# Optimization experiments

Hardware: AMD Instinct MI355X
Metric: run time of the kernel (lower is better)

Reference implementation:

```python
import jax, jax.numpy as jnp
import numpy as np

N = 50000      # number of nodes (rows of edge_embeddings)
E = 800000     # number of edges
D = 256        # edge_dim
TOPK = 50


def setup_inputs() -> dict:
    key = jax.random.key(0)
    k1, k2, k3, k4, k5, k6 = jax.random.split(key, 6)
    edge_embeddings = jax.random.normal(k1, (N, D), dtype=jnp.float32)
    edge_index = jax.random.randint(k2, (2, E), 0, N, dtype=jnp.int64)
    # PyTorch nn.Linear default init: U(-1/sqrt(fan_in), 1/sqrt(fan_in))
    s1 = 1.0 / np.sqrt(2 * D)
    s2 = 1.0 / np.sqrt(D)
    W1 = jax.random.uniform(k3, (2 * D, D), jnp.float32, -s1, s1)
    b1 = jax.random.uniform(k4, (D,), jnp.float32, -s1, s1)
    W2 = jax.random.uniform(k5, (D, 1), jnp.float32, -s2, s2)
    b2 = jax.random.uniform(k6, (1,), jnp.float32, -s2, s2)
    return {"edge_embeddings": edge_embeddings, "W1": W1, "b1": b1,
            "W2": W2, "b2": b2, "edge_index": edge_index, "top_k": TOPK}


def reference(edge_embeddings, W1, b1, W2, b2, edge_index, top_k):
    src, dst = edge_index[0], edge_index[1]           # [E]
    valid = src < dst                                  # original keeps only i<j pairs
    # gather + concat: [E, 2D]
    pair_emb = jnp.concatenate([edge_embeddings[src], edge_embeddings[dst]], axis=-1)
    h = jax.nn.relu(pair_emb @ W1 + b1)                # [E, D]
    score = jax.nn.sigmoid(h @ W2 + b2)[:, 0]          # [E], in (0,1)
    # invalid edges get score -1 (< any sigmoid output) so topk picks only valid ones
    masked = jnp.where(valid, score, jnp.float32(-1.0))
    top_scores, top_idx = jax.lax.top_k(masked, top_k)
    top_pairs = edge_index[:, top_idx]                 # [2, k] (src,dst) of top edges
    return top_pairs, top_scores
```

## Files before the change

### kernel.cpp

```cpp
#include <hip/hip_runtime.h>
#include <hip/hip_bf16.h>
#include <cstdint>

#define TOPK 50
#define CANDS 400
#define HIST_BINS 16384
#define CAND_CAP 16384
#define NFBLK 512
#define SORT_CAP 8192

typedef __attribute__((ext_vector_type(8))) short bf16x8;
typedef __attribute__((ext_vector_type(4))) float f32x4;

__device__ __forceinline__ unsigned short f2bf(float f) {
    unsigned u = __float_as_uint(f);
    u += 0x7FFFu + ((u >> 16) & 1u);
    return (unsigned short)(u >> 16);
}

__global__ __launch_bounds__(256) void prep_count(const float* __restrict__ W1,
                                                  unsigned* __restrict__ Wcf4,
                                                  unsigned* __restrict__ hist,
                                                  unsigned* __restrict__ misc,
                                                  const int* __restrict__ eidx,
                                                  unsigned* __restrict__ bcount, int E) {
    __shared__ int s_is64;
    if (threadIdx.x == 0) {
        int allz = 1;
        for (int q = 0; q < 64; ++q)
            if (eidx[2 * q + 1] != 0) { allz = 0; break; }
        s_is64 = allz;
    }
    __syncthreads();
    const int is64 = s_is64;

    int g = blockIdx.x * blockDim.x + threadIdx.x;
    if (g < 256 * 64) {
        int l = g & 63;
        int kt = (g >> 6) & 7;
        int nt = g >> 9;
        int col = nt * 16 + (l & 15);
        int kb = kt * 32 + (l >> 4) * 8;
        unsigned short h[8];
#pragma unroll
        for (int j = 0; j < 8; ++j) {
            int k = kb + j;
            float f = (col < 256) ? W1[k * 256 + col] : W1[(256 + k) * 256 + (col - 256)];
            h[j] = f2bf(f);
        }
        unsigned* dst = Wcf4 + (size_t)g * 4;
        dst[0] = (unsigned)h[0] | ((unsigned)h[1] << 16);
        dst[1] = (unsigned)h[2] | ((unsigned)h[3] << 16);
        dst[2] = (unsigned)h[4] | ((unsigned)h[5] << 16);
        dst[3] = (unsigned)h[6] | ((unsigned)h[7] << 16);
    }
    if (g < HIST_BINS) hist[g] = 0;
    if (g == 0) {
        misc[0] = (unsigned)is64;
        misc[2] = 0;
        misc[3] = 0;
        misc[4] = 0;
    }

    const int chunk = (E + gridDim.x - 1) / gridDim.x;
    const int lo = blockIdx.x * chunk;
    const int hi = min(E, lo + chunk);
    unsigned cnt = 0;
    for (int e = lo + threadIdx.x; e < hi; e += blockDim.x) {
        int s, d;
        if (is64) {
            s = ((const int2*)eidx)[e].x;
            d = ((const int2*)eidx)[(size_t)e + E].x;
        } else {
            s = eidx[e];
            d = eidx[e + E];
        }
        cnt += (s < d);
    }
#pragma unroll
    for (int off = 32; off; off >>= 1) cnt += __shfl_xor(cnt, off, 64);
    __shared__ unsigned wsum[4];
    if ((threadIdx.x & 63) == 0) wsum[threadIdx.x >> 6] = cnt;
    __syncthreads();
    if (threadIdx.x == 0)
        bcount[blockIdx.x] = wsum[0] + wsum[1] + wsum[2] + wsum[3];
}

__global__ __launch_bounds__(256) void gemm_fused(const float* __restrict__ emb,
                                                  const bf16x8* __restrict__ Bv,
                                                  const float* __restrict__ b1,
                                                  unsigned char* __restrict__ C8, int M) {
    __shared__ uint4 afrag[2048];
    const int t = threadIdx.x;
    const int w = t >> 6;
    const int l = t & 63;

    uint2* w2 = (uint2*)afrag;
#pragma unroll
    for (int iter = 0; iter < 16; ++iter) {
        int r = iter * 4 + w;
        int c0 = l * 4;
        int gr = blockIdx.x * 64 + r;
        float4 v = make_float4(0.f, 0.f, 0.f, 0.f);
        if (gr < M) v = *(const float4*)&emb[(size_t)gr * 256 + c0];
        unsigned u0 = (unsigned)f2bf(v.x) | ((unsigned)f2bf(v.y) << 16);
        unsigned u1 = (unsigned)f2bf(v.z) | ((unsigned)f2bf(v.w) << 16);
        int mt = r >> 4;
        int kt = c0 >> 5;
        int lane = (r & 15) + ((c0 & 31) >> 3) * 16;
        int f = mt * 8 + kt;
        int slot = f * 64 + (lane ^ (f & 7));
        w2[slot * 2 + ((c0 & 7) >> 2)] = make_uint2(u0, u1);
    }
    __syncthreads();

    const int wn = w;
#pragma unroll
    for (int nh = 0; nh < 2; ++nh) {
        f32x4 acc[4][4];
#pragma unroll
        for (int i = 0; i < 4; ++i)
#pragma unroll
            for (int j = 0; j < 4; ++j) acc[i][j] = (f32x4){0.f, 0.f, 0.f, 0.f};

        const int nt0 = wn * 8 + nh * 4;
        bf16x8 bcur[4];
#pragma unroll
        for (int j = 0; j < 4; ++j)
            bcur[j] = Bv[(size_t)((nt0 + j) * 8 + 0) * 64 + l];

#pragma unroll
        for (int kt = 0; kt < 8; ++kt) {
            bf16x8 af[4];
#pragma unroll
            for (int i = 0; i < 4; ++i)
                af[i] = *(const bf16x8*)&afrag[(i * 8 + kt) * 64 + (l ^ kt)];
            bf16x8 bnxt[4];
            if (kt < 7) {
#pragma unroll
                for (int j = 0; j < 4; ++j)
                    bnxt[j] = Bv[(size_t)((nt0 + j) * 8 + kt + 1) * 64 + l];
            }
#pragma unroll
            for (int i = 0; i < 4; ++i)
#pragma unroll
                for (int j = 0; j < 4; ++j)
                    acc[i][j] = __builtin_amdgcn_mfma_f32_16x16x32_bf16(af[i], bcur[j], acc[i][j], 0, 0, 0);
            if (kt < 7) {
#pragma unroll
                for (int j = 0; j < 4; ++j) bcur[j] = bnxt[j];
            }
        }

#pragma unroll
        for (int i = 0; i < 4; ++i) {
            int row0 = blockIdx.x * 64 + i * 16 + (l >> 4) * 4;
#pragma unroll
            for (int j = 0; j < 4; ++j) {
                int col = (nt0 + j) * 16 + (l & 15);
                float bias = (col < 256) ? b1[col] : 0.f;
#pragma unroll
                for (int r = 0; r < 4; ++r) {
                    float v = acc[i][j][r] + bias;
                    int pk = __builtin_amdgcn_cvt_pk_fp8_f32(v, v, 0, false);
                    C8[(size_t)(row0 + r) * 512 + col] = (unsigned char)(pk & 0xFF);
                }
            }
        }
    }
}

__global__ __launch_bounds__(256) void write_valid_scan(const int* __restrict__ eidx,
                                                        unsigned* __restrict__ misc,
                                                        const unsigned* __restrict__ bcount,
                                                        int* __restrict__ vsrc,
                                                        int* __restrict__ vdst,
                                                        int* __restrict__ vid, int E) {
    const int is64 = (int)misc[0];
    const int bid = blockIdx.x;
    const int t = threadIdx.x;
    __shared__ unsigned red[256];

    unsigned c0 = bcount[t], c1 = bcount[t + 256];
    unsigned pa = ((t < bid) ? c0 : 0u) + ((t + 256 < bid) ? c1 : 0u);
    red[t] = pa;
    __syncthreads();
    for (int s = 128; s; s >>= 1) {
        if (t < s) red[t] += red[t + s];
        __syncthreads();
    }
    const unsigned myoff = red[0];
    __syncthreads();
    red[t] = c0 + c1;
    __syncthreads();
    for (int s = 128; s; s >>= 1) {
        if (t < s) red[t] += red[t + s];
        __syncthreads();
    }
    if (bid == 0 && t == 0) misc[4] = red[0];

    const int chunk = (E + gridDim.x - 1) / gridDim.x;
    const int lo = bid * chunk;
    const int hi = min(E, lo + chunk);
    const int lane = t & 63;
    const int w = t >> 6;
    __shared__ unsigned wcnt[4];
    unsigned running = myoff;
    for (int base = lo; base < hi; base += blockDim.x) {
        int e = base + t;
        bool valid = false;
        int s = 0, d = 0;
        if (e < hi) {
            if (is64) {
                s = ((const int2*)eidx)[e].x;
                d = ((const int2*)eidx)[(size_t)e + E].x;
            } else {
                s = eidx[e];
                d = eidx[e + E];
            }
            valid = s < d;
        }
        unsigned long long m = __ballot(valid);
        unsigned pfx = __popcll(m & ((1ull << lane) - 1ull));
        if (lane == 0) wcnt[w] = __popcll(m);
        __syncthreads();
        unsigned wbase = running;
        for (int i = 0; i < w; ++i) wbase += wcnt[i];
        if (valid) {
            unsigned p = wbase + pfx;
            vsrc[p] = s;
            vdst[p] = d;
            vid[p] = e;
        }
        unsigned tot = wcnt[0] + wcnt[1] + wcnt[2] + wcnt[3];
        __syncthreads();
        running += tot;
    }
}

__device__ __forceinline__ float dotq(unsigned a, unsigned b, float4 w) {
    float s;
    s  = fmaxf(__builtin_amdgcn_cvt_f32_fp8(a, 0) + __builtin_amdgcn_cvt_f32_fp8(b, 0), 0.f) * w.x;
    s += fmaxf(__builtin_amdgcn_cvt_f32_fp8(a, 1) + __builtin_amdgcn_cvt_f32_fp8(b, 1), 0.f) * w.y;
    s += fmaxf(__builtin_amdgcn_cvt_f32_fp8(a, 2) + __builtin_amdgcn_cvt_f32_fp8(b, 2), 0.f) * w.z;
    s += fmaxf(__builtin_amdgcn_cvt_f32_fp8(a, 3) + __builtin_amdgcn_cvt_f32_fp8(b, 3), 0.f) * w.w;
    return s;
}

__global__ __launch_bounds__(256) void edge_score_fp8(const unsigned char* __restrict__ C8,
                                                      const int* __restrict__ vsrc,
                                                      const int* __restrict__ vdst,
                                                      const float* __restrict__ W2,
                                                      const float* __restrict__ b2,
                                                      float* __restrict__ svals,
                                                      const unsigned* __restrict__ misc) {
    const int V = (int)misc[4];
    const int lane = threadIdx.x & 63;
    const int q = lane & 15;
    const int g = lane >> 4;
    const int wid = blockIdx.x * (blockDim.x >> 6) + (threadIdx.x >> 6);
    const int nw = gridDim.x * (blockDim.x >> 6);

    const float4 w0 = *(const float4*)&W2[q * 16 + 0];
    const float4 w1 = *(const float4*)&W2[q * 16 + 4];
    const float4 w2 = *(const float4*)&W2[q * 16 + 8];
    const float4 w3 = *(const float4*)&W2[q * 16 + 12];
    const float bb2 = b2[0];

    for (int base = wid * 4; base < V; base += nw * 4) {
        const int slot = base + g;
        const bool ok = slot < V;
        const int src = ok ? vsrc[slot] : 0;
        const int dst = ok ? vdst[slot] : 0;
        const uint4 ua = *(const uint4*)(C8 + (size_t)src * 512 + q * 16);
        const uint4 ub = *(const uint4*)(C8 + (size_t)dst * 512 + 256 + q * 16);
        float p = dotq(ua.x, ub.x, w0);
        p += dotq(ua.y, ub.y, w1);
        p += dotq(ua.z, ub.z, w2);
        p += dotq(ua.w, ub.w, w3);
        p += __shfl_xor(p, 1, 64);
        p += __shfl_xor(p, 2, 64);
        p += __shfl_xor(p, 4, 64);
        p += __shfl_xor(p, 8, 64);
        if (q == 0 && ok) {
            float z = p + bb2;
            float sc = 1.0f / (1.0f + expf(-z));
            svals[slot] = sc;
        }
    }
}

__global__ __launch_bounds__(256) void hist_kernel(const float* __restrict__ svals,
                                                   const unsigned* __restrict__ misc,
                                                   unsigned* __restrict__ hist) {
    __shared__ unsigned lh[HIST_BINS];
    const int V = (int)misc[4];
    const int t = threadIdx.x;
    for (int i = t; i < HIST_BINS; i += 256) lh[i] = 0;
    __syncthreads();
    int i = blockIdx.x * blockDim.x + t;
    int stride = gridDim.x * blockDim.x;
    for (int v = i; v < V; v += stride)
        atomicAdd(&lh[__float_as_uint(svals[v]) >> 16], 1u);
    __syncthreads();
    for (int b = t; b < HIST_BINS; b += 256) {
        unsigned c = lh[b];
        if (c) atomicAdd(&hist[b], c);
    }
}

__global__ __launch_bounds__(256) void compact(const float* __restrict__ svals,
                                               const int* __restrict__ vid,
                                               const unsigned* __restrict__ hist,
                                               unsigned* __restrict__ misc,
                                               unsigned long long* __restrict__ cand) {
    __shared__ unsigned chunk[256];
    __shared__ unsigned s_thr;
    const int t = threadIdx.x;
    {
        unsigned s = 0;
        for (int i = 0; i < 64; ++i) s += hist[t * 64 + i];
        chunk[t] = s;
    }
    __syncthreads();
    if (t == 0) {
        unsigned cum = 0;
        int c;
        unsigned thr = 0;
        for (c = 255; c >= 0; --c) {
            if (cum + chunk[c] >= CANDS) break;
            cum += chunk[c];
        }
        if (c >= 0) {
            for (int b = c * 64 + 63; b >= c * 64; --b) {
                cum += hist[b];
                if (cum >= CANDS) { thr = ((unsigned)b) << 16; break; }
            }
        }
        s_thr = thr;
    }
    __syncthreads();
    const unsigned thr = s_thr;

    const int V = (int)misc[4];
    int i = blockIdx.x * blockDim.x + t;
    int stride = gridDim.x * blockDim.x;
    for (int v = i; v < V; v += stride) {
        unsigned bits = __float_as_uint(svals[v]);
        if (bits >= thr) {
            unsigned pos = atomicAdd(&misc[3], 1u);
            if (pos < CAND_CAP)
                cand[pos] = ((unsigned long long)bits << 32) |
                            (unsigned)(0xFFFFFFFFu - (unsigned)vid[v]);
        }
    }
}

__global__ __launch_bounds__(256) void rescore(const float* __restrict__ emb,
                                               const float* __restrict__ W1,
                                               const float* __restrict__ b1,
                                               const float* __restrict__ W2,
                                               const float* __restrict__ b2,
                                               const int* __restrict__ eidx,
                                               const unsigned long long* __restrict__ cand,
                                               const unsigned* __restrict__ misc,
                                               unsigned long long* __restrict__ rescored,
                                               int E) {
    __shared__ float es[256], ed[256];
    __shared__ float red[256];
    const int C = (int)min(misc[3], (unsigned)CAND_CAP);
    const int is64 = (int)misc[0];
    const int t = threadIdx.x;
    for (int c = blockIdx.x; c < C; c += gridDim.x) {
        unsigned long long entry = cand[c];
        unsigned e = 0xFFFFFFFFu - (unsigned)(entry & 0xFFFFFFFFu);
        int src, dst;
        if (is64) {
            src = eidx[2 * (size_t)e];
            dst = eidx[2 * ((size_t)e + E)];
        } else {
            src = eidx[e];
            dst = eidx[e + E];
        }
        es[t] = emb[(size_t)src * 256 + t];
        ed[t] = emb[(size_t)dst * 256 + t];
        __syncthreads();
        float h = b1[t];
#pragma unroll 8
        for (int k = 0; k < 256; ++k) h += es[k] * W1[k * 256 + t];
#pragma unroll 8
        for (int k = 0; k < 256; ++k) h += ed[k] * W1[(256 + k) * 256 + t];
        red[t] = fmaxf(h, 0.f) * W2[t];
        __syncthreads();
        for (int s = 128; s; s >>= 1) {
            if (t < s) red[t] += red[t + s];
            __syncthreads();
        }
        if (t == 0) {
            float z = red[0] + b2[0];
            float sc = 1.0f / (1.0f + expf(-z));
            rescored[c] = ((unsigned long long)__float_as_uint(sc) << 32) |
                          (unsigned)(0xFFFFFFFFu - e);
        }
        __syncthreads();
    }
}

__global__ __launch_bounds__(256) void final_topk(unsigned long long* __restrict__ rescored,
                                                  const unsigned* __restrict__ misc,
                                                  const int* __restrict__ eidx,
                                                  float* __restrict__ out, int E) {
    __shared__ unsigned long long a[SORT_CAP];
    const int t = threadIdx.x;
    const int C = (int)min(misc[3], (unsigned)CAND_CAP);
    const int is64 = (int)misc[0];

    if (C <= SORT_CAP) {
        int n = 256;
        while (n < C) n <<= 1;
        for (int i = t; i < n; i += 256) a[i] = (i < C) ? rescored[i] : 0ull;
        __syncthreads();
        for (int k = 2; k <= n; k <<= 1) {
            for (int j = k >> 1; j > 0; j >>= 1) {
                for (int i = t; i < n; i += 256) {
                    int ixj = i ^ j;
                    if (ixj > i) {
                        unsigned long long x = a[i], y = a[ixj];
                        bool sw = ((i & k) == 0) ? (x < y) : (x > y);
                        if (sw) { a[i] = y; a[ixj] = x; }
                    }
                }
                __syncthreads();
            }
        }
        if (t < TOPK) {
            unsigned long long m = a[t];
            if (m != 0ull) {
                unsigned bits = (unsigned)(m >> 32);
                unsigned e = 0xFFFFFFFFu - (unsigned)(m & 0xFFFFFFFFu);
                int src, dst;
                if (is64) {
                    src = eidx[2 * (size_t)e];
                    dst = eidx[2 * ((size_t)e + E)];
                } else {
                    src = eidx[e];
                    dst = eidx[e + E];
                }
                out[t] = (float)src;
                out[TOPK + t] = (float)dst;
                out[2 * TOPK + t] = __uint_as_float(bits);
            } else {
                out[t] = -1.f;
                out[TOPK + t] = -1.f;
                out[2 * TOPK + t] = -1.f;
            }
        }
        return;
    }

    __shared__ unsigned long long red[256];
    for (int r = 0; r < TOPK; ++r) {
        unsigned long long best = 0ull;
        for (int i = t; i < C; i += 256) {
            unsigned long long v = rescored[i];
            if (v > best) best = v;
        }
        red[t] = best;
        __syncthreads();
        for (int s = 128; s; s >>= 1) {
            if (t < s) {
                if (red[t + s] > red[t]) red[t] = red[t + s];
            }
            __syncthreads();
        }
        unsigned long long m = red[0];
        __syncthreads();
        for (int i = t; i < C; i += 256)
            if (rescored[i] == m) rescored[i] = 0ull;
        if (t == 0) {
            if (m != 0ull) {
                unsigned bits = (unsigned)(m >> 32);
                unsigned e = 0xFFFFFFFFu - (unsigned)(m & 0xFFFFFFFFu);
                int src, dst;
                if (is64) {
                    src = eidx[2 * (size_t)e];
                    dst = eidx[2 * ((size_t)e + E)];
                } else {
                    src = eidx[e];
                    dst = eidx[e + E];
                }
                out[r] = (float)src;
                out[TOPK + r] = (float)dst;
                out[2 * TOPK + r] = __uint_as_float(bits);
            } else {
                out[r] = -1.f;
                out[TOPK + r] = -1.f;
                out[2 * TOPK + r] = -1.f;
            }
        }
        __syncthreads();
    }
}

extern "C" void kernel_launch(void* const* d_in, const int* in_sizes, int n_in,
                              void* d_out, int out_size, void* d_ws, size_t ws_size,
                              hipStream_t stream) {
    const float* emb = (const float*)d_in[0];
    const float* W1  = (const float*)d_in[1];
    const float* b1  = (const float*)d_in[2];
    const float* W2  = (const float*)d_in[3];
    const float* b2  = (const float*)d_in[4];
    const int*   eidx = (const int*)d_in[5];

    const int M = in_sizes[0] / 256;
    const int E = in_sizes[5] / 2;
    const int Mpad = ((M + 63) / 64) * 64;

    char* p = (char*)d_ws;
    auto alloc = [&](size_t bytes) {
        char* r = p;
        p += (bytes + 255) & ~(size_t)255;
        return r;
    };
    unsigned* Wcf4 = (unsigned*)alloc(256 * 512 * 2);
    unsigned char* C8 = (unsigned char*)alloc((size_t)Mpad * 512);
    float* svals = (float*)alloc((size_t)E * 4);
    int* vsrc = (int*)alloc((size_t)E * 4);
    int* vdst = (int*)alloc((size_t)E * 4);
    int* vid  = (int*)alloc((size_t)E * 4);
    unsigned* hist = (unsigned*)alloc(HIST_BINS * 4);
    unsigned long long* cand = (unsigned long long*)alloc(CAND_CAP * 8);
    unsigned long long* resc = (unsigned long long*)alloc(CAND_CAP * 8);
    unsigned* bcount = (unsigned*)alloc(NFBLK * 4);
    unsigned* misc = (unsigned*)alloc(256);

    float* out = (float*)d_out;

    prep_count<<<NFBLK, 256, 0, stream>>>(W1, Wcf4, hist, misc, eidx, bcount, E);

    gemm_fused<<<Mpad / 64, 256, 0, stream>>>(emb, (const bf16x8*)Wcf4, b1, C8, M);

    write_valid_scan<<<NFBLK, 256, 0, stream>>>(eidx, misc, bcount, vsrc, vdst, vid, E);

    edge_score_fp8<<<2048, 256, 0, stream>>>(C8, vsrc, vdst, W2, b2, svals, misc);

    hist_kernel<<<128, 256, 0, stream>>>(svals, misc, hist);

    compact<<<512, 256, 0, stream>>>(svals, vid, hist, misc, cand);

    rescore<<<1024, 256, 0, stream>>>(emb, W1, b1, W2, b2, eidx, cand, misc, resc, E);

    final_topk<<<1, 256, 0, stream>>>(resc, misc, eidx, out, E);
}
```

Before: 150.8 us.

## Merge GEMM and valid-edge scan into one launch; subsample score histogram

Combines the bf16 MFMA GEMM and the valid-edge compaction scan into a single launch, with the first blocks doing the GEMM and the rest doing the scan. This removes one kernel launch and lets the two independent stages overlap. The histogram now samples every 8th score and uses a threshold rank of 64 among the samples instead of 400 among all scores, which cuts histogram atomic work. The cost is that the candidate threshold becomes statistical, so the candidate count varies and could overflow the cap or miss true top-k entries if the sampling is unrepresentative.

```diff
diff --git a/kernel.cpp b/kernel.cpp
--- a/kernel.cpp
+++ b/kernel.cpp
@@ -3,7 +3,8 @@
 #include <cstdint>
 
 #define TOPK 50
-#define CANDS 400
+#define SUB_RANK 64
+#define HIST_STRIDE 8
 #define HIST_BINS 16384
 #define CAND_CAP 16384
 #define NFBLK 512
@@ -86,155 +87,157 @@
         bcount[blockIdx.x] = wsum[0] + wsum[1] + wsum[2] + wsum[3];
 }
 
-__global__ __launch_bounds__(256) void gemm_fused(const float* __restrict__ emb,
-                                                  const bf16x8* __restrict__ Bv,
-                                                  const float* __restrict__ b1,
-                                                  unsigned char* __restrict__ C8, int M) {
+__global__ __launch_bounds__(256) void gemm_plus_write(const float* __restrict__ emb,
+                                                       const bf16x8* __restrict__ Bv,
+                                                       const float* __restrict__ b1,
+                                                       unsigned char* __restrict__ C8,
+                                                       int M, int NG,
+                                                       const int* __restrict__ eidx,
+                                                       unsigned* __restrict__ misc,
+                                                       const unsigned* __restrict__ bcount,
+                                                       int* __restrict__ vsrc,
+                                                       int* __restrict__ vdst,
+                                                       int* __restrict__ vid, int E) {
     __shared__ uint4 afrag[2048];
     const int t = threadIdx.x;
-    const int w = t >> 6;
-    const int l = t & 63;
-
-    uint2* w2 = (uint2*)afrag;
-#pragma unroll
-    for (int iter = 0; iter < 16; ++iter) {
-        int r = iter * 4 + w;
-        int c0 = l * 4;
-        int gr = blockIdx.x * 64 + r;
-        float4 v = make_float4(0.f, 0.f, 0.f, 0.f);
-        if (gr < M) v = *(const float4*)&emb[(size_t)gr * 256 + c0];
-        unsigned u0 = (unsigned)f2bf(v.x) | ((unsigned)f2bf(v.y) << 16);
-        unsigned u1 = (unsigned)f2bf(v.z) | ((unsigned)f2bf(v.w) << 16);
-        int mt = r >> 4;
-        int kt = c0 >> 5;
-        int lane = (r & 15) + ((c0 & 31) >> 3) * 16;
-        int f = mt * 8 + kt;
-        int slot = f * 64 + (lane ^ (f & 7));
-        w2[slot * 2 + ((c0 & 7) >> 2)] = make_uint2(u0, u1);
-    }
-    __syncthreads();
-
-    const int wn = w;
-#pragma unroll
-    for (int nh = 0; nh < 2; ++nh) {
-        f32x4 acc[4][4];
-#pragma unroll
-        for (int i = 0; i < 4; ++i)
-#pragma unroll
-            for (int j = 0; j < 4; ++j) acc[i][j] = (f32x4){0.f, 0.f, 0.f, 0.f};
-
-        const int nt0 = wn * 8 + nh * 4;
-        bf16x8 bcur[4];
-#pragma unroll
-        for (int j = 0; j < 4; ++j)
-            bcur[j] = Bv[(size_t)((nt0 + j) * 8 + 0) * 64 + l];
-
-#pragma unroll
-        for (int kt = 0; kt < 8; ++kt) {
-            bf16x8 af[4];
+
+    if ((int)blockIdx.x < NG) {
+        const int w = t >> 6;
+        const int l = t & 63;
+
+        uint2* w2 = (uint2*)afrag;
+#pragma unroll
+        for (int iter = 0; iter < 16; ++iter) {
+            int r = iter * 4 + w;
+            int c0 = l * 4;
+            int gr = blockIdx.x * 64 + r;
+            float4 v = make_float4(0.f, 0.f, 0.f, 0.f);
+            if (gr < M) v = *(const float4*)&emb[(size_t)gr * 256 + c0];
+            unsigned u0 = (unsigned)f2bf(v.x) | ((unsigned)f2bf(v.y) << 16);
+            unsigned u1 = (unsigned)f2bf(v.z) | ((unsigned)f2bf(v.w) << 16);
+            int mt = r >> 4;
+            int kt = c0 >> 5;
+            int lane = (r & 15) + ((c0 & 31) >> 3) * 16;
+            int f = mt * 8 + kt;
+            int slot = f * 64 + (lane ^ (f & 7));
+            w2[slot * 2 + ((c0 & 7) >> 2)] = make_uint2(u0, u1);
+        }
+        __syncthreads();
+
+        const int wn = w;
+#pragma unroll
+        for (int nh = 0; nh < 2; ++nh) {
+            f32x4 acc[4][4];
 #pragma unroll
             for (int i = 0; i < 4; ++i)
-                af[i] = *(const bf16x8*)&afrag[(i * 8 + kt) * 64 + (l ^ kt)];
-            bf16x8 bnxt[4];
-            if (kt < 7) {
-#pragma unroll
-                for (int j = 0; j < 4; ++j)
-                    bnxt[j] = Bv[(size_t)((nt0 + j) * 8 + kt + 1) * 64 + l];
-            }
-#pragma unroll
-            for (int i = 0; i < 4; ++i)
-#pragma unroll
-                for (int j = 0; j < 4; ++j)
-                    acc[i][j] = __builtin_amdgcn_mfma_f32_16x16x32_bf16(af[i], bcur[j], acc[i][j], 0, 0, 0);
-            if (kt < 7) {
-#pragma unroll
-                for (int j = 0; j < 4; ++j) bcur[j] = bnxt[j];
-            }
-        }
-
-#pragma unroll
-        for (int i = 0; i < 4; ++i) {
-            int row0 = blockIdx.x * 64 + i * 16 + (l >> 4) * 4;
-#pragma unroll
-            for (int j = 0; j < 4; ++j) {
-                int col = (nt0 + j) * 16 + (l & 15);
-                float bias = (col < 256) ? b1[col] : 0.f;
-#pragma unroll
-                for (int r = 0; r < 4; ++r) {
-                    float v = acc[i][j][r] + bias;
-                    int pk = __builtin_amdgcn_cvt_pk_fp8_f32(v, v, 0, false);
-                    C8[(size_t)(row0 + r) * 512 + col] = (unsigned char)(pk & 0xFF);
-                }
-            }
-        }
-    }
-}
-
-__global__ __launch_bounds__(256) void write_valid_scan(const int* __restrict__ eidx,
-                                                        unsigned* __restrict__ misc,
-                                                        const unsigned* __restrict__ bcount,
-                                                        int* __restrict__ vsrc,
-                                                        int* __restrict__ vdst,
-                                                        int* __restrict__ vid, int E) {
-    const int is64 = (int)misc[0];
-    const int bid = blockIdx.x;
-    const int t = threadIdx.x;
-    __shared__ unsigned red[256];
-
-    unsigned c0 = bcount[t], c1 = bcount[t + 256];
-    unsigned pa = ((t < bid) ? c0 : 0u) + ((t + 256 < bid) ? c1 : 0u);
-    red[t] = pa;
-    __syncthreads();
-    for (int s = 128; s; s >>= 1) {
-        if (t < s) red[t] += red[t + s];
-        __syncthreads();
-    }
-    const unsigned myoff = red[0];
-    __syncthreads();
-    red[t] = c0 + c1;
-    __syncthreads();
-    for (int s = 128; s; s >>= 1) {
-        if (t < s) red[t] += red[t + s];
-        __syncthreads();
-    }
-    if (bid == 0 && t == 0) misc[4] = red[0];
-
-    const int chunk = (E + gridDim.x - 1) / gridDim.x;
-    const int lo = bid * chunk;
-    const int hi = min(E, lo + chunk);
-    const int lane = t & 63;
-    const int w = t >> 6;
-    __shared__ unsigned wcnt[4];
-    unsigned running = myoff;
-    for (int base = lo; base < hi; base += blockDim.x) {
-        int e = base + t;
-        bool valid = false;
-        int s = 0, d = 0;
-        if (e < hi) {
-            if (is64) {
-                s = ((const int2*)eidx)[e].x;
-                d = ((const int2*)eidx)[(size_t)e + E].x;
-            } else {
-                s = eidx[e];
-                d = eidx[e + E];
-            }
-            valid = s < d;
-        }
-        unsigned long long m = __ballot(valid);
-        unsigned pfx = __popcll(m & ((1ull << lane) - 1ull));
-        if (lane == 0) wcnt[w] = __popcll(m);
-        __syncthreads();
-        unsigned wbase = running;
-        for (int i = 0; i < w; ++i) wbase += wcnt[i];
-        if (valid) {
-            unsigned p = wbase + pfx;
-            vsrc[p] = s;
-            vdst[p] = d;
-            vid[p] = e;
-        }
-        unsigned tot = wcnt[0] + wcnt[1] + wcnt[2] + wcnt[3];
-        __syncthreads();
-        running += tot;
+#pragma unroll
+                for (int j = 0; j < 4; ++j) acc[i][j] = (f32x4){0.f, 0.f, 0.f, 0.f};
+
+            const int nt0 = wn * 8 + nh * 4;
+            bf16x8 bcur[4];
+#pragma unroll
+            for (int j = 0; j < 4; ++j)
+                bcur[j] = Bv[(size_t)((nt0 + j) * 8 + 0) * 64 + l];
+
+#pragma unroll
+            for (int kt = 0; kt < 8; ++kt) {
+                bf16x8 af[4];
+#pragma unroll
+                for (int i = 0; i < 4; ++i)
+                    af[i] = *(const bf16x8*)&afrag[(i * 8 + kt) * 64 + (l ^ kt)];
+                bf16x8 bnxt[4];
+                if (kt < 7) {
+#pragma unroll
+                    for (int j = 0; j < 4; ++j)
+                        bnxt[j] = Bv[(size_t)((nt0 + j) * 8 + kt + 1) * 64 + l];
+                }
+#pragma unroll
+                for (int i = 0; i < 4; ++i)
+#pragma unroll
+                    for (int j = 0; j < 4; ++j)
+                        acc[i][j] = __builtin_amdgcn_mfma_f32_16x16x32_bf16(af[i], bcur[j], acc[i][j], 0, 0, 0);
+                if (kt < 7) {
+#pragma unroll
+                    for (int j = 0; j < 4; ++j) bcur[j] = bnxt[j];
+                }
+            }
+
+#pragma unroll
+            for (int i = 0; i < 4; ++i) {
+                int row0 = blockIdx.x * 64 + i * 16 + (l >> 4) * 4;
+#pragma unroll
+                for (int j = 0; j < 4; ++j) {
+                    int col = (nt0 + j) * 16 + (l & 15);
+                    float bias = (col < 256) ? b1[col] : 0.f;
+#pragma unroll
+                    for (int r = 0; r < 4; ++r) {
+                        float v = acc[i][j][r] + bias;
+                        int pk = __builtin_amdgcn_cvt_pk_fp8_f32(v, v, 0, false);
+                        C8[(size_t)(row0 + r) * 512 + col] = (unsigned char)(pk & 0xFF);
+                    }
+                }
+            }
+        }
+    } else {
+        const int is64 = (int)misc[0];
+        const int bid = (int)blockIdx.x - NG;
+        unsigned* red = (unsigned*)afrag;
+        unsigned* wcnt = red + 256;
+
+        unsigned c0 = bcount[t], c1 = bcount[t + 256];
+        unsigned pa = ((t < bid) ? c0 : 0u) + ((t + 256 < bid) ? c1 : 0u);
+        red[t] = pa;
+        __syncthreads();
+        for (int s = 128; s; s >>= 1) {
+            if (t < s) red[t] += red[t + s];
+            __syncthreads();
+        }
+        const unsigned myoff = red[0];
+        __syncthreads();
+        red[t] = c0 + c1;
+        __syncthreads();
+        for (int s = 128; s; s >>= 1) {
+            if (t < s) red[t] += red[t + s];
+            __syncthreads();
+        }
+        if (bid == 0 && t == 0) misc[4] = red[0];
+
+        const int chunk = (E + NFBLK - 1) / NFBLK;
+        const int lo = bid * chunk;
+        const int hi = min(E, lo + chunk);
+        const int lane = t & 63;
+        const int w = t >> 6;
+        unsigned running = myoff;
+        for (int base = lo; base < hi; base += blockDim.x) {
+            int e = base + t;
+            bool valid = false;
+            int s = 0, d = 0;
+            if (e < hi) {
+                if (is64) {
+                    s = ((const int2*)eidx)[e].x;
+                    d = ((const int2*)eidx)[(size_t)e + E].x;
+                } else {
+                    s = eidx[e];
+                    d = eidx[e + E];
+                }
+                valid = s < d;
+            }
+            unsigned long long m = __ballot(valid);
+            unsigned pfx = __popcll(m & ((1ull << lane) - 1ull));
+            if (lane == 0) wcnt[w] = __popcll(m);
+            __syncthreads();
+            unsigned wbase = running;
+            for (int i = 0; i < w; ++i) wbase += wcnt[i];
+            if (valid) {
+                unsigned p = wbase + pfx;
+                vsrc[p] = s;
+                vdst[p] = d;
+                vid[p] = e;
+            }
+            unsigned tot = wcnt[0] + wcnt[1] + wcnt[2] + wcnt[3];
+            __syncthreads();
+            running += tot;
+        }
     }
 }
 
@@ -294,14 +297,14 @@
                                                    const unsigned* __restrict__ misc,
                                                    unsigned* __restrict__ hist) {
     __shared__ unsigned lh[HIST_BINS];
-    const int V = (int)misc[4];
+    const int V = (int)misc[4] / HIST_STRIDE;
     const int t = threadIdx.x;
     for (int i = t; i < HIST_BINS; i += 256) lh[i] = 0;
     __syncthreads();
     int i = blockIdx.x * blockDim.x + t;
     int stride = gridDim.x * blockDim.x;
     for (int v = i; v < V; v += stride)
-        atomicAdd(&lh[__float_as_uint(svals[v]) >> 16], 1u);
+        atomicAdd(&lh[__float_as_uint(svals[(size_t)v * HIST_STRIDE]) >> 16], 1u);
     __syncthreads();
     for (int b = t; b < HIST_BINS; b += 256) {
         unsigned c = lh[b];
@@ -328,13 +331,13 @@
         int c;
         unsigned thr = 0;
         for (c = 255; c >= 0; --c) {
-            if (cum + chunk[c] >= CANDS) break;
+            if (cum + chunk[c] >= SUB_RANK) break;
             cum += chunk[c];
         }
         if (c >= 0) {
             for (int b = c * 64 + 63; b >= c * 64; --b) {
                 cum += hist[b];
-                if (cum >= CANDS) { thr = ((unsigned)b) << 16; break; }
+                if (cum >= SUB_RANK) { thr = ((unsigned)b) << 16; break; }
             }
         }
         s_thr = thr;
@@ -515,6 +518,7 @@
     const int M = in_sizes[0] / 256;
     const int E = in_sizes[5] / 2;
     const int Mpad = ((M + 63) / 64) * 64;
+    const int NG = Mpad / 64;
 
     char* p = (char*)d_ws;
     auto alloc = [&](size_t bytes) {
@@ -538,9 +542,9 @@
 
     prep_count<<<NFBLK, 256, 0, stream>>>(W1, Wcf4, hist, misc, eidx, bcount, E);
 
-    gemm_fused<<<Mpad / 64, 256, 0, stream>>>(emb, (const bf16x8*)Wcf4, b1, C8, M);
-
-    write_valid_scan<<<NFBLK, 256, 0, stream>>>(eidx, misc, bcount, vsrc, vdst, vid, E);
+    gemm_plus_write<<<NG + NFBLK, 256, 0, stream>>>(emb, (const bf16x8*)Wcf4, b1, C8,
+                                                    M, NG, eidx, misc, bcount,
+                                                    vsrc, vdst, vid, E);
 
     edge_score_fp8<<<2048, 256, 0, stream>>>(C8, vsrc, vdst, W2, b2, svals, misc);
 
```

Result: faster. 142.4 us (-5.6%).
